# Performance work log

Hardware: AMD Instinct MI355X
Metric: run time of the kernel (lower is better)

## Reference

```python
import jax, jax.numpy as jnp
import numpy as np
import math

B, T, C, H = 8, 1024, 512, 8
D = C // H
PAD = 64  # last PAD key positions are padding


def setup_inputs() -> dict:
    key = jax.random.key(0)
    ks = jax.random.split(key, 11)
    s = 1.0 / math.sqrt(C)
    x = jax.random.normal(ks[0], (B, T, C), dtype=jnp.float32)
    attn_bias = jax.random.normal(ks[1], (B, H, T, T), dtype=jnp.float32)
    # True = padding; mask out the last PAD key positions
    key_padding_mask = jnp.broadcast_to(jnp.arange(T) >= (T - PAD), (B, T))
    Wq = jax.random.normal(ks[2], (C, C), dtype=jnp.float32) * s
    bq = jnp.zeros((C,), dtype=jnp.float32)
    Wk = jax.random.normal(ks[3], (C, C), dtype=jnp.float32) * s
    bk = jnp.zeros((C,), dtype=jnp.float32)
    Wv = jax.random.normal(ks[4], (C, C), dtype=jnp.float32) * s
    bv = jnp.zeros((C,), dtype=jnp.float32)
    Wo = jax.random.normal(ks[5], (C, C), dtype=jnp.float32) * s
    bo = jnp.zeros((C,), dtype=jnp.float32)
    return {"x": x, "attn_bias": attn_bias, "key_padding_mask": key_padding_mask,
            "Wq": Wq, "bq": bq, "Wk": Wk, "bk": bk, "Wv": Wv, "bv": bv,
            "Wo": Wo, "bo": bo}


def reference(x, attn_bias, key_padding_mask, Wq, bq, Wk, bk, Wv, bv, Wo, bo):
    scale = math.sqrt(D)
    q = (x @ Wq.T + bq).reshape(B, T, H, D)
    k = (x @ Wk.T + bk).reshape(B, T, H, D)
    v = (x @ Wv.T + bv).reshape(B, T, H, D)
    # scores: (B, H, Tq, Tk)
    scores = jnp.einsum('bqhd,bkhd->bhqk', q, k) / scale + attn_bias
    scores = jnp.where(key_padding_mask[:, None, None, :], -jnp.inf, scores)
    attn = jax.nn.softmax(scores, axis=-1)
    out = jnp.einsum('bhqk,bkhd->bqhd', attn, v).reshape(B, T, C)
    return out @ Wo.T + bo
```

## Files before the change

kernel.cpp:

```cpp
#include <hip/hip_runtime.h>

#define B_   8
#define T_   1024
#define C_   512
#define H_   8
#define D_   64
#define TKV_ 960

typedef short short8 __attribute__((ext_vector_type(8)));
typedef float f32x4  __attribute__((ext_vector_type(4)));
typedef unsigned short u16;

__device__ __forceinline__ u16 f2bf(float f) {
    unsigned int u = __builtin_bit_cast(unsigned int, f);
    u += 0x7fffu + ((u >> 16) & 1u);
    return (u16)(u >> 16);
}
__device__ __forceinline__ float bf2f(u16 h) {
    unsigned int u = ((unsigned int)h) << 16;
    return __builtin_bit_cast(float, u);
}
__device__ __forceinline__ u16 f2bf_rn(float f) {
    unsigned int u = __builtin_bit_cast(unsigned int, f);
    return (u16)((u + 0x8000u) >> 16);
}

#define MFMA(a, b, c) __builtin_amdgcn_mfma_f32_16x16x32_bf16((a), (b), (c), 0, 0, 0)

__device__ __forceinline__ void gl16(const u16* g, u16* l) {
    __builtin_amdgcn_global_load_lds(
        reinterpret_cast<const __attribute__((address_space(1))) unsigned int*>(
            (unsigned long long)g),
        reinterpret_cast<__attribute__((address_space(3))) unsigned int*>(
            (unsigned int)(unsigned long long)l),
        16, 0, 0);
}

__global__ __launch_bounds__(256) void prep_kernel(
    const float* __restrict__ x,
    const float* __restrict__ Wq, const float* __restrict__ Wk,
    const float* __restrict__ Wv, const float* __restrict__ Wo,
    const float* __restrict__ bq, const float* __restrict__ bk, const float* __restrict__ bv,
    u16* __restrict__ xh,
    u16* __restrict__ wh, u16* __restrict__ wl,
    u16* __restrict__ woh, u16* __restrict__ wol,
    float* __restrict__ bqkv)
{
    const int bx = blockIdx.x, tid = threadIdx.x;
    if (bx < 4096) {
        int e = (bx * 256 + tid) * 4;
        float4 v = *(const float4*)(x + e);
        ushort4 h;
        h.x = f2bf(v.x); h.y = f2bf(v.y); h.z = f2bf(v.z); h.w = f2bf(v.w);
        *(ushort4*)(xh + e) = h;
    } else if (bx < 5120) {
        int seg = (bx - 4096) >> 8;
        int e = ((bx - 4096) & 255) * 1024 + tid * 4;
        const float* src = (seg == 0) ? Wq : (seg == 1) ? Wk : (seg == 2) ? Wv : Wo;
        float4 v = *(const float4*)(src + e);
        ushort4 h, lo;
        h.x = f2bf(v.x); lo.x = f2bf(v.x - bf2f(h.x));
        h.y = f2bf(v.y); lo.y = f2bf(v.y - bf2f(h.y));
        h.z = f2bf(v.z); lo.z = f2bf(v.z - bf2f(h.z));
        h.w = f2bf(v.w); lo.w = f2bf(v.w - bf2f(h.w));
        if (seg < 3) {
            *(ushort4*)(wh + seg * 262144 + e) = h;
            *(ushort4*)(wl + seg * 262144 + e) = lo;
        } else {
            *(ushort4*)(woh + e) = h;
            *(ushort4*)(wol + e) = lo;
        }
    } else {
        for (int e = tid; e < 1536; e += 256) {
            bqkv[e] = (e < 512) ? bq[e] : (e < 1024) ? bk[e - 512] : bv[e - 1024];
        }
    }
}

__global__ __launch_bounds__(256) void qkv_gemm_kernel(
    const u16* __restrict__ xh,
    const u16* __restrict__ wh, const u16* __restrict__ wl,
    const float* __restrict__ bqkv,
    u16* __restrict__ qo, u16* __restrict__ ko, u16* __restrict__ vt)
{
    __shared__ __align__(16) u16 Ah[128 * 32], Bh[128 * 32], Bl[128 * 32];
    const int m0 = blockIdx.x * 128;
    const int n0 = blockIdx.y * 128;
    const int tid = threadIdx.x;
    const int wv = tid >> 6, lane = tid & 63, quad = lane >> 4, l16 = lane & 15;
    const int wm = (wv & 1) * 64, wn = (wv >> 1) * 64;

    const int srow = wv * 16 + (lane >> 2);
    const int scol = (lane & 3) * 8;
    const u16* a0p = xh + (size_t)(m0 + srow) * C_ + scol;
    const u16* b0h = wh + (size_t)(n0 + srow) * C_ + scol;
    const u16* b0l = wl + (size_t)(n0 + srow) * C_ + scol;
    u16* ldsA  = Ah + wv * 512;
    u16* ldsBh = Bh + wv * 512;
    u16* ldsBl = Bl + wv * 512;

    f32x4 acc[4][4];
    #pragma unroll
    for (int i = 0; i < 4; ++i)
        #pragma unroll
        for (int j = 0; j < 4; ++j)
            acc[i][j] = (f32x4){0.f, 0.f, 0.f, 0.f};

    for (int kt = 0; kt < C_; kt += 32) {
        __syncthreads();
        gl16(a0p + kt,            ldsA);
        gl16(a0p + kt + 64 * C_,  ldsA + 2048);
        gl16(b0h + kt,            ldsBh);
        gl16(b0h + kt + 64 * C_,  ldsBh + 2048);
        gl16(b0l + kt,            ldsBl);
        gl16(b0l + kt + 64 * C_,  ldsBl + 2048);
        __syncthreads();

        short8 ah[4];
        #pragma unroll
        for (int i = 0; i < 4; ++i)
            ah[i] = *(const short8*)(Ah + (wm + i * 16 + l16) * 32 + quad * 8);
        #pragma unroll
        for (int j = 0; j < 4; ++j) {
            short8 bhj = *(const short8*)(Bh + (wn + j * 16 + l16) * 32 + quad * 8);
            short8 blj = *(const short8*)(Bl + (wn + j * 16 + l16) * 32 + quad * 8);
            #pragma unroll
            for (int i = 0; i < 4; ++i) {
                acc[i][j] = MFMA(ah[i], bhj, acc[i][j]);
                acc[i][j] = MFMA(ah[i], blj, acc[i][j]);
            }
        }
    }

    const int mat = n0 >> 9;
    #pragma unroll
    for (int j = 0; j < 4; ++j) {
        const int ng = n0 + wn + j * 16 + l16;
        const float bias = bqkv[ng];
        const int idx = ng & 511;
        const int h = idx >> 6, d = idx & 63;
        #pragma unroll
        for (int i = 0; i < 4; ++i) {
            const int mg = m0 + wm + i * 16 + quad * 4;
            const int b = mg >> 10, t = mg & 1023;
            if (mat == 2) {
                ushort4 us;
                us.x = f2bf(acc[i][j][0] + bias);
                us.y = f2bf(acc[i][j][1] + bias);
                us.z = f2bf(acc[i][j][2] + bias);
                us.w = f2bf(acc[i][j][3] + bias);
                *(ushort4*)(vt + ((size_t)(b * H_ + h) * D_ + d) * T_ + t) = us;
            } else {
                u16* dst = (mat == 0) ? qo : ko;
                #pragma unroll
                for (int r = 0; r < 4; ++r)
                    dst[((size_t)(b * H_ + h) * T_ + t + r) * D_ + d] = f2bf(acc[i][j][r] + bias);
            }
        }
    }
}

__global__ __launch_bounds__(256) void attn_kernel(
    const u16* __restrict__ q, const u16* __restrict__ k, const u16* __restrict__ vt,
    const float* __restrict__ bias, u16* __restrict__ ao)
{
    __shared__ __align__(16) u16 Ks[64 * 72], Vs[64 * 72], Ps[64 * 72];
    const int q0 = blockIdx.x * 64;
    const int bh = blockIdx.y;
    const int tid = threadIdx.x;
    const int wv = tid >> 6, lane = tid & 63, quad = lane >> 4, l16 = lane & 15;
    const int sr = tid >> 3;
    const int sc = (tid & 7) * 8;

    const size_t qbase = ((size_t)bh * T_ + q0 + wv * 16 + l16) * D_ + quad * 8;
    const short8 qa0 = *(const short8*)(q + qbase);
    const short8 qa1 = *(const short8*)(q + qbase + 32);

    float l_part[4] = {0.f, 0.f, 0.f, 0.f};
    f32x4 O[4];
    #pragma unroll
    for (int dt = 0; dt < 4; ++dt) O[dt] = (f32x4){0.f, 0.f, 0.f, 0.f};

    const int qrow = q0 + wv * 16 + quad * 4;
    const float* __restrict__ brow = bias + ((size_t)bh * T_ + qrow) * T_;

    const u16* kp = k  + ((size_t)bh * T_ + sr) * D_ + sc;
    const u16* vp = vt + ((size_t)bh * D_ + sr) * T_ + sc;

    short8 kv0 = *(const short8*)(kp);
    short8 kv1 = *(const short8*)(kp + (size_t)32 * D_);
    short8 vv0 = *(const short8*)(vp);
    short8 vv1 = *(const short8*)(vp + (size_t)32 * T_);
    float bb[4][4];
    #pragma unroll
    for (int nt = 0; nt < 4; ++nt)
        #pragma unroll
        for (int r = 0; r < 4; ++r)
            bb[nt][r] = brow[(size_t)r * T_ + nt * 16 + l16];

    for (int k0 = 0; k0 < TKV_; k0 += 64) {
        __syncthreads();
        *(short8*)(Ks + (sr     ) * 72 + sc) = kv0;
        *(short8*)(Ks + (sr + 32) * 72 + sc) = kv1;
        *(short8*)(Vs + (sr     ) * 72 + sc) = vv0;
        *(short8*)(Vs + (sr + 32) * 72 + sc) = vv1;
        __syncthreads();

        const int kn = k0 + 64;
        short8 nk0, nk1, nv0, nv1;
        float bn[4][4];
        if (kn < TKV_) {
            nk0 = *(const short8*)(kp + (size_t)kn * D_);
            nk1 = *(const short8*)(kp + (size_t)(kn + 32) * D_);
            nv0 = *(const short8*)(vp + kn);
            nv1 = *(const short8*)(vp + (size_t)32 * T_ + kn);
            #pragma unroll
            for (int nt = 0; nt < 4; ++nt)
                #pragma unroll
                for (int r = 0; r < 4; ++r)
                    bn[nt][r] = brow[(size_t)r * T_ + kn + nt * 16 + l16];
        }

        f32x4 S[4];
        #pragma unroll
        for (int nt = 0; nt < 4; ++nt) S[nt] = (f32x4){0.f, 0.f, 0.f, 0.f};
        #pragma unroll
        for (int c = 0; c < 2; ++c) {
            const short8 qa = c ? qa1 : qa0;
            #pragma unroll
            for (int nt = 0; nt < 4; ++nt) {
                short8 kb = *(const short8*)(Ks + (nt * 16 + l16) * 72 + c * 32 + quad * 8);
                S[nt] = MFMA(qa, kb, S[nt]);
            }
        }

        #pragma unroll
        for (int nt = 0; nt < 4; ++nt) {
            #pragma unroll
            for (int r = 0; r < 4; ++r) {
                float p = __expf(fmaf(S[nt][r], 0.125f, bb[nt][r]));
                l_part[r] += p;
                Ps[(wv * 16 + (r & 1) * 8 + quad * 2 + (r >> 1)) * 72 + nt * 16 + l16] =
                    f2bf_rn(p);
            }
        }

        #pragma unroll
        for (int c = 0; c < 2; ++c) {
            short8 pa = *(const short8*)(Ps + (wv * 16 + (l16 & 1) * 8 + (l16 >> 1)) * 72
                                            + c * 32 + quad * 8);
            #pragma unroll
            for (int dt = 0; dt < 4; ++dt) {
                short8 vb = *(const short8*)(Vs + (dt * 16 + l16) * 72 + c * 32 + quad * 8);
                O[dt] = MFMA(pa, vb, O[dt]);
            }
        }

        if (kn < TKV_) {
            kv0 = nk0; kv1 = nk1; vv0 = nv0; vv1 = nv1;
            #pragma unroll
            for (int nt = 0; nt < 4; ++nt)
                #pragma unroll
                for (int r = 0; r < 4; ++r)
                    bb[nt][r] = bn[nt][r];
        }
    }

    float l_i[4];
    #pragma unroll
    for (int r = 0; r < 4; ++r) {
        float rs = l_part[r];
        #pragma unroll
        for (int off = 1; off < 16; off <<= 1) rs += __shfl_xor(rs, off, 16);
        l_i[r] = rs;
    }

    const int b = bh >> 3, h = bh & 7;
    #pragma unroll
    for (int r = 0; r < 4; ++r) {
        const float inv = 1.0f / l_i[r];
        #pragma unroll
        for (int dt = 0; dt < 4; ++dt)
            ao[((size_t)b * T_ + qrow + r) * C_ + h * D_ + dt * 16 + l16] =
                f2bf(O[dt][r] * inv);
    }
}

__global__ __launch_bounds__(256) void o_gemm_kernel(
    const u16* __restrict__ ao,
    const u16* __restrict__ woh, const u16* __restrict__ wol,
    const float* __restrict__ bo, float* __restrict__ out)
{
    __shared__ __align__(16) u16 Ah[128 * 32], Bh[64 * 32], Bl[64 * 32];
    const int m0 = blockIdx.x * 128;
    const int n0 = blockIdx.y * 64;
    const int tid = threadIdx.x;
    const int wv = tid >> 6, lane = tid & 63, quad = lane >> 4, l16 = lane & 15;
    const int wm = (wv & 1) * 64, wn = (wv >> 1) * 32;

    const int srow = wv * 16 + (lane >> 2);
    const int scol = (lane & 3) * 8;
    const u16* ap  = ao  + (size_t)(m0 + srow) * C_ + scol;
    const u16* bph = woh + (size_t)(n0 + srow) * C_ + scol;
    const u16* bpl = wol + (size_t)(n0 + srow) * C_ + scol;
    u16* ldsA  = Ah + wv * 512;
    u16* ldsBh = Bh + wv * 512;
    u16* ldsBl = Bl + wv * 512;

    f32x4 acc[4][2];
    #pragma unroll
    for (int i = 0; i < 4; ++i)
        #pragma unroll
        for (int j = 0; j < 2; ++j)
            acc[i][j] = (f32x4){0.f, 0.f, 0.f, 0.f};

    for (int kt = 0; kt < C_; kt += 32) {
        __syncthreads();
        gl16(ap + kt,           ldsA);
        gl16(ap + kt + 64 * C_, ldsA + 2048);
        gl16(bph + kt,          ldsBh);
        gl16(bpl + kt,          ldsBl);
        __syncthreads();

        short8 ah[4];
        #pragma unroll
        for (int i = 0; i < 4; ++i)
            ah[i] = *(const short8*)(Ah + (wm + i * 16 + l16) * 32 + quad * 8);
        #pragma unroll
        for (int j = 0; j < 2; ++j) {
            short8 bhj = *(const short8*)(Bh + (wn + j * 16 + l16) * 32 + quad * 8);
            short8 blj = *(const short8*)(Bl + (wn + j * 16 + l16) * 32 + quad * 8);
            #pragma unroll
            for (int i = 0; i < 4; ++i) {
                acc[i][j] = MFMA(ah[i], bhj, acc[i][j]);
                acc[i][j] = MFMA(ah[i], blj, acc[i][j]);
            }
        }
    }

    #pragma unroll
    for (int j = 0; j < 2; ++j) {
        const int ng = n0 + wn + j * 16 + l16;
        const float bias = bo[ng];
        #pragma unroll
        for (int i = 0; i < 4; ++i) {
            const int mg = m0 + wm + i * 16 + quad * 4;
            #pragma unroll
            for (int r = 0; r < 4; ++r)
                out[(size_t)(mg + r) * C_ + ng] = acc[i][j][r] + bias;
        }
    }
}

extern "C" void kernel_launch(void* const* d_in, const int* in_sizes, int n_in,
                              void* d_out, int out_size, void* d_ws, size_t ws_size,
                              hipStream_t stream) {
    const float* x    = (const float*)d_in[0];
    const float* bias = (const float*)d_in[1];
    const float* Wq = (const float*)d_in[3];
    const float* bq = (const float*)d_in[4];
    const float* Wk = (const float*)d_in[5];
    const float* bk = (const float*)d_in[6];
    const float* Wv = (const float*)d_in[7];
    const float* bv = (const float*)d_in[8];
    const float* Wo = (const float*)d_in[9];
    const float* bo = (const float*)d_in[10];
    float* out = (float*)d_out;

    char* ws = (char*)d_ws;
    u16*   xh   = (u16*)(ws + 0);
    u16*   wh   = (u16*)(ws + 8388608);
    u16*   wl   = (u16*)(ws + 9961472);
    u16*   woh  = (u16*)(ws + 11534336);
    u16*   wol  = (u16*)(ws + 12058624);
    u16*   qb   = (u16*)(ws + 12582912);
    u16*   kb   = (u16*)(ws + 20971520);
    u16*   vtb  = (u16*)(ws + 29360128);
    u16*   aob  = (u16*)(ws + 37748736);
    float* bqkv = (float*)(ws + 46137344);

    prep_kernel<<<dim3(5121), 256, 0, stream>>>(x, Wq, Wk, Wv, Wo, bq, bk, bv,
                                                xh, wh, wl, woh, wol, bqkv);
    qkv_gemm_kernel<<<dim3(64, 12), 256, 0, stream>>>(xh, wh, wl, bqkv, qb, kb, vtb);
    attn_kernel<<<dim3(16, 64), 256, 0, stream>>>(qb, kb, vtb, bias, aob);
    o_gemm_kernel<<<dim3(64, 8), 256, 0, stream>>>(aob, woh, wol, bo, out);
}
```

Baseline: 466.7 us.

## Remap blocks per XCD, load bias in-iteration, add MFMA priority hints

All three kernels remap the linear block id so consecutive blocks sent to the same XCD share operand tiles (same M rows for GEMMs, same batch-head for attention), aiming at better L2 reuse across the 8 XCDs. The attention kernel now loads the bias tile inside each iteration instead of prefetching it one step ahead, which cuts register pressure. It also wraps the MFMA sections in s_setprio so waves issuing matrix ops get scheduling priority. The risk is that bias load latency is now exposed within the iteration, and the remapping assumes the grid dimensions match the hardcoded constants.

```diff
diff --git a/kernel.cpp b/kernel.cpp
--- a/kernel.cpp
+++ b/kernel.cpp
@@ -84,8 +84,10 @@
     u16* __restrict__ qo, u16* __restrict__ ko, u16* __restrict__ vt)
 {
     __shared__ __align__(16) u16 Ah[128 * 32], Bh[128 * 32], Bl[128 * 32];
-    const int m0 = blockIdx.x * 128;
-    const int n0 = blockIdx.y * 128;
+    const int id = blockIdx.y * 64 + blockIdx.x;
+    const int xcd = id & 7, local = id >> 3;
+    const int m0 = (xcd * 8 + local / 12) * 128;
+    const int n0 = (local % 12) * 128;
     const int tid = threadIdx.x;
     const int wv = tid >> 6, lane = tid & 63, quad = lane >> 4, l16 = lane & 15;
     const int wm = (wv & 1) * 64, wn = (wv >> 1) * 64;
@@ -165,8 +167,10 @@
     const float* __restrict__ bias, u16* __restrict__ ao)
 {
     __shared__ __align__(16) u16 Ks[64 * 72], Vs[64 * 72], Ps[64 * 72];
-    const int q0 = blockIdx.x * 64;
-    const int bh = blockIdx.y;
+    const int id  = blockIdx.y * 16 + blockIdx.x;
+    const int nid = (id & 7) * 128 + (id >> 3);
+    const int bh  = nid >> 4;
+    const int q0  = (nid & 15) * 64;
     const int tid = threadIdx.x;
     const int wv = tid >> 6, lane = tid & 63, quad = lane >> 4, l16 = lane & 15;
     const int sr = tid >> 3;
@@ -191,12 +195,6 @@
     short8 kv1 = *(const short8*)(kp + (size_t)32 * D_);
     short8 vv0 = *(const short8*)(vp);
     short8 vv1 = *(const short8*)(vp + (size_t)32 * T_);
-    float bb[4][4];
-    #pragma unroll
-    for (int nt = 0; nt < 4; ++nt)
-        #pragma unroll
-        for (int r = 0; r < 4; ++r)
-            bb[nt][r] = brow[(size_t)r * T_ + nt * 16 + l16];
 
     for (int k0 = 0; k0 < TKV_; k0 += 64) {
         __syncthreads();
@@ -208,22 +206,24 @@
 
         const int kn = k0 + 64;
         short8 nk0, nk1, nv0, nv1;
-        float bn[4][4];
         if (kn < TKV_) {
             nk0 = *(const short8*)(kp + (size_t)kn * D_);
             nk1 = *(const short8*)(kp + (size_t)(kn + 32) * D_);
             nv0 = *(const short8*)(vp + kn);
             nv1 = *(const short8*)(vp + (size_t)32 * T_ + kn);
-            #pragma unroll
-            for (int nt = 0; nt < 4; ++nt)
-                #pragma unroll
-                for (int r = 0; r < 4; ++r)
-                    bn[nt][r] = brow[(size_t)r * T_ + kn + nt * 16 + l16];
-        }
+        }
+
+        float bb[4][4];
+        #pragma unroll
+        for (int nt = 0; nt < 4; ++nt)
+            #pragma unroll
+            for (int r = 0; r < 4; ++r)
+                bb[nt][r] = brow[(size_t)r * T_ + k0 + nt * 16 + l16];
 
         f32x4 S[4];
         #pragma unroll
         for (int nt = 0; nt < 4; ++nt) S[nt] = (f32x4){0.f, 0.f, 0.f, 0.f};
+        __builtin_amdgcn_s_setprio(1);
         #pragma unroll
         for (int c = 0; c < 2; ++c) {
             const short8 qa = c ? qa1 : qa0;
@@ -233,6 +233,7 @@
                 S[nt] = MFMA(qa, kb, S[nt]);
             }
         }
+        __builtin_amdgcn_s_setprio(0);
 
         #pragma unroll
         for (int nt = 0; nt < 4; ++nt) {
@@ -245,6 +246,7 @@
             }
         }
 
+        __builtin_amdgcn_s_setprio(1);
         #pragma unroll
         for (int c = 0; c < 2; ++c) {
             short8 pa = *(const short8*)(Ps + (wv * 16 + (l16 & 1) * 8 + (l16 >> 1)) * 72
@@ -255,15 +257,9 @@
                 O[dt] = MFMA(pa, vb, O[dt]);
             }
         }
-
-        if (kn < TKV_) {
-            kv0 = nk0; kv1 = nk1; vv0 = nv0; vv1 = nv1;
-            #pragma unroll
-            for (int nt = 0; nt < 4; ++nt)
-                #pragma unroll
-                for (int r = 0; r < 4; ++r)
-                    bb[nt][r] = bn[nt][r];
-        }
+        __builtin_amdgcn_s_setprio(0);
+
+        if (kn < TKV_) { kv0 = nk0; kv1 = nk1; vv0 = nv0; vv1 = nv1; }
     }
 
     float l_i[4];
@@ -292,8 +288,10 @@
     const float* __restrict__ bo, float* __restrict__ out)
 {
     __shared__ __align__(16) u16 Ah[128 * 32], Bh[64 * 32], Bl[64 * 32];
-    const int m0 = blockIdx.x * 128;
-    const int n0 = blockIdx.y * 64;
+    const int id = blockIdx.y * 64 + blockIdx.x;
+    const int xcd = id & 7, local = id >> 3;
+    const int m0 = (xcd * 8 + local / 8) * 128;
+    const int n0 = (local % 8) * 64;
     const int tid = threadIdx.x;
     const int wv = tid >> 6, lane = tid & 63, quad = lane >> 4, l16 = lane & 15;
     const int wm = (wv & 1) * 64, wn = (wv >> 1) * 32;
```

Result: no change. 461.4 us (-1.1%).
